# Optimization experiments

Hardware: AMD Instinct MI355X
Metric: run time of the kernel (lower is better)

## Reference

```python
import jax, jax.numpy as jnp
import numpy as np
from jax import lax

K = 3
K2 = K * K
PAD = 1          # dcn padding = kernel_size // 2
OFF_DIL = 2      # offset conv dilation & padding
GN_GROUPS = 32
EPS = 1e-5


def setup_inputs() -> dict:
    key = jax.random.key(0)
    ks = jax.random.split(key, 4)
    B, C1, C2, H, W = 4, 256, 256, 64, 64
    x = jax.random.normal(ks[0], (B, C1, H, W), jnp.float32)
    # offset conv params (zero-init in module; small random here so deformable
    # sampling is genuinely irregular)
    w_off = jax.random.normal(ks[1], (3 * K2, C1, K, K), jnp.float32) * 0.01
    b_off = jax.random.normal(ks[2], (3 * K2,), jnp.float32) * 0.01
    # dcn weight, bias=False
    w_dcn = jax.random.normal(ks[3], (C2, C1, K, K), jnp.float32) * (1.0 / np.sqrt(C1 * K2))
    gamma = jnp.ones((C2,), jnp.float32)
    beta = jnp.zeros((C2,), jnp.float32)
    return {"x": x, "w_off": w_off, "b_off": b_off, "w_dcn": w_dcn,
            "gamma": gamma, "beta": beta}


def _dcnv2_block(x, w_off, b_off, w_dcn, gamma, beta):
    B, C, H, W = x.shape
    C2 = w_dcn.shape[0]

    # ---- offset/mask prediction: 3x3 conv, dilation=2, padding=2, stride=1 ----
    out_off = lax.conv_general_dilated(
        x, w_off, window_strides=(1, 1), padding=[(OFF_DIL, OFF_DIL)] * 2,
        rhs_dilation=(OFF_DIL, OFF_DIL),
        dimension_numbers=("NCHW", "OIHW", "NCHW"))
    out_off = out_off + b_off[None, :, None, None]

    offset = jnp.nan_to_num(jnp.clip(out_off[:, :2 * K2], -64.0, 64.0))
    mask = jax.nn.sigmoid(out_off[:, 2 * K2:])                     # [B,K2,H,W]

    off = offset.reshape(B, K2, 2, H, W)                            # (dy,dx) pairs per kernel pt
    dy, dx = off[:, :, 0], off[:, :, 1]                             # [B,K2,H,W]

    # ---- sampling positions: p0 + pk + offset (stride=1, pad=1, dil=1) ----
    ii = (jnp.arange(K2) // K).astype(jnp.float32)                  # kernel row
    jj = (jnp.arange(K2) % K).astype(jnp.float32)                   # kernel col
    yo = jnp.arange(H, dtype=jnp.float32)
    xo = jnp.arange(W, dtype=jnp.float32)
    py = yo[None, None, :, None] - PAD + ii[None, :, None, None] + dy   # [B,K2,H,W]
    px = xo[None, None, None, :] - PAD + jj[None, :, None, None] + dx

    y0 = jnp.floor(py)
    x0 = jnp.floor(px)
    wy = py - y0                                                    # frac weights
    wx = px - x0
    y0i = y0.astype(jnp.int32)
    x0i = x0.astype(jnp.int32)

    xf = x.reshape(B, C, H * W)

    def gather(yi, xi):
        # zero outside image (torchvision zero-padding bilinear semantics)
        valid = (yi >= 0) & (yi < H) & (xi >= 0) & (xi < W)
        idx = jnp.clip(yi, 0, H - 1) * W + jnp.clip(xi, 0, W - 1)   # [B,K2,H,W]
        v = jax.vmap(lambda xb, ib: xb[:, ib])(xf, idx.reshape(B, -1))  # [B,C,K2*H*W]
        v = v.reshape(B, C, K2, H, W)
        return v * valid[:, None].astype(x.dtype)

    v00 = gather(y0i, x0i)
    v01 = gather(y0i, x0i + 1)
    v10 = gather(y0i + 1, x0i)
    v11 = gather(y0i + 1, x0i + 1)

    wy_ = wy[:, None]
    wx_ = wx[:, None]
    samp = (v00 * (1 - wy_) * (1 - wx_) + v01 * (1 - wy_) * wx_
            + v10 * wy_ * (1 - wx_) + v11 * wy_ * wx_)              # [B,C,K2,H,W]
    samp = samp * mask[:, None]                                     # modulated (DCNv2)

    out = jnp.einsum("bckhw,dck->bdhw", samp, w_dcn.reshape(C2, C, K2))

    # ---- GroupNorm(32, C2) + SiLU ----
    G = GN_GROUPS
    o = out.reshape(B, G, C2 // G, H, W)
    mu = o.mean(axis=(2, 3, 4), keepdims=True)
    var = o.var(axis=(2, 3, 4), keepdims=True)
    o = (o - mu) * lax.rsqrt(var + EPS)
    out = o.reshape(B, C2, H, W) * gamma[None, :, None, None] + beta[None, :, None, None]
    return out * jax.nn.sigmoid(out)


def reference(x, w_off, b_off, w_dcn, gamma, beta):
    return _dcnv2_block(x, w_off, b_off, w_dcn, gamma, beta)
```

## Files before the change

kernel.cpp:

```cpp
#include <hip/hip_runtime.h>
#include <math.h>

#define HW 4096

typedef __attribute__((ext_vector_type(8))) short short8;
typedef __attribute__((ext_vector_type(4))) float f32x4;

static __device__ inline ushort f2bf(float f) {
    uint u = __builtin_bit_cast(uint, f);
    return (ushort)((u + 0x7fffu + ((u >> 16) & 1u)) >> 16);
}
static __device__ inline float lof(uint u) { return __builtin_bit_cast(float, u << 16); }
static __device__ inline float hif(uint u) { return __builtin_bit_cast(float, u & 0xffff0000u); }

__global__ __launch_bounds__(256) void k0_xt(const float* __restrict__ x, ushort* __restrict__ xt)
{
    const int blk = blockIdx.x;
    const int b = blk >> 7, h = (blk & 127) >> 1, ch = blk & 1;
    __shared__ ushort tile[64 * 130];
    const float* xb = x + ((size_t)(b * 256 + ch * 128)) * HW + h * 64;
    const int t = threadIdx.x;
    for (int e = t; e < 8192; e += 256) {
        const int c = e >> 6, j = e & 63;
        tile[j * 130 + c] = f2bf(xb[c * HW + j]);
    }
    __syncthreads();
    for (int e = t; e < 4096; e += 256) {
        const int j = e >> 6, q = e & 63;
        uint* xo = (uint*)(xt + ((size_t)b * HW + h * 64 + j) * 256 + ch * 128);
        xo[q] = *(const uint*)&tile[j * 130 + 2 * q];
    }
}

__global__ __launch_bounds__(256) void k0_w(const float* __restrict__ w_dcn,
    const float* __restrict__ w_off, ushort* __restrict__ wT, ushort* __restrict__ wA)
{
    const int bid = blockIdx.x;
    const int t = threadIdx.x;
    if (bid < 256) {
        const int d = bid;
        __shared__ float wl[2304];
        for (int i = t; i < 2304; i += 256) wl[i] = w_dcn[d * 2304 + i];
        __syncthreads();
        for (int i = t; i < 2304; i += 256) {
            const int k = i >> 8, c = i & 255;
            wT[k * 65536 + d * 256 + c] = f2bf(wl[c * 9 + k]);
        }
    } else {
        const int e = (bid - 256) * 256 + t;
        const int k = e >> 13, r = e & 8191;
        const int oc = r >> 8, c = r & 255;
        wA[e] = f2bf(oc < 27 ? w_off[(oc * 256 + c) * 9 + k] : 0.f);
    }
}

__global__ __launch_bounds__(512) void k1_mfma(const ushort* __restrict__ xt,
    const ushort* __restrict__ wA, const float* __restrict__ b_off,
    float* __restrict__ offs, float* __restrict__ mk)
{
    const int bid = blockIdx.x;
    const int b = bid >> 7, rr_ = bid & 127, h = rr_ >> 1, wh = rr_ & 1;
    const int t = threadIdx.x;
    const int lane = t & 63, wv = t >> 6;
    const int wq = wv & 1, cq = wv >> 1;
    const int n = lane & 15, kq = lane >> 4;
    __shared__ float red[2][3][64][8];

    f32x4 acc0 = {0.f, 0.f, 0.f, 0.f}, acc1 = {0.f, 0.f, 0.f, 0.f};
    const ushort* xb = xt + ((size_t)b * HW) * 256;
    const int wcol = wh * 32 + wq * 16 + n;
    const int cb = cq * 64 + kq * 8;

#pragma unroll
    for (int k = 0; k < 9; ++k) {
        const int i = k / 3, j = k % 3;
        const int hh = h + 2 * (i - 1);
        const int ww = wcol + 2 * (j - 1);
        const bool ok = ((unsigned)hh < 64u) && ((unsigned)ww < 64u);
        const int hc = min(max(hh, 0), 63), wc = min(max(ww, 0), 63);
        const ushort* xrow = xb + (hc * 64 + wc) * 256 + cb;
        const ushort* wr0 = wA + (k * 32 + n) * 256 + cb;
#pragma unroll
        for (int c0 = 0; c0 < 64; c0 += 32) {
            short8 bv = *(const short8*)(xrow + c0);
            if (!ok) bv = (short8){0, 0, 0, 0, 0, 0, 0, 0};
            const short8 a0 = *(const short8*)(wr0 + c0);
            const short8 a1 = *(const short8*)(wr0 + 16 * 256 + c0);
            acc0 = __builtin_amdgcn_mfma_f32_16x16x32_bf16(a0, bv, acc0, 0, 0, 0);
            acc1 = __builtin_amdgcn_mfma_f32_16x16x32_bf16(a1, bv, acc1, 0, 0, 0);
        }
    }

    if (cq > 0) {
#pragma unroll
        for (int r = 0; r < 4; ++r) {
            red[wq][cq - 1][lane][r]     = acc0[r];
            red[wq][cq - 1][lane][4 + r] = acc1[r];
        }
    }
    __syncthreads();
    if (cq == 0) {
#pragma unroll
        for (int p = 0; p < 3; ++p)
#pragma unroll
            for (int r = 0; r < 4; ++r) {
                acc0[r] += red[wq][p][lane][r];
                acc1[r] += red[wq][p][lane][4 + r];
            }
        const int hw = h * 64 + wcol;
#pragma unroll
        for (int r = 0; r < 4; ++r) {
            {
                const int oc = kq * 4 + r;
                float v = acc0[r] + b_off[oc];
                v = fminf(fmaxf(v, -64.f), 64.f);
                offs[(b * 18 + oc) * HW + hw] = v;
            }
            {
                const int oc = 16 + kq * 4 + r;
                const float v = acc1[r] + b_off[min(oc, 26)];
                if (oc < 18) {
                    offs[(b * 18 + oc) * HW + hw] = fminf(fmaxf(v, -64.f), 64.f);
                } else if (oc < 27) {
                    mk[(b * 9 + (oc - 18)) * HW + hw] = 1.f / (1.f + expf(-v));
                }
            }
        }
    }
}

__global__ __launch_bounds__(256) void k2_dcn(const ushort* __restrict__ xt, const ushort* __restrict__ wT,
    const float* __restrict__ offs, const float* __restrict__ mk, float* __restrict__ out)
{
    const int bid = blockIdx.x;
    const int wg = (bid & 7) * 64 + (bid >> 3);
    const int b = wg >> 7, h = (wg & 127) >> 1, wh = wg & 1;
    const int t = threadIdx.x;
    const int lane = t & 63, wv = t >> 6;
    const int n0 = lane & 15, kq = lane >> 4;
    const int d0 = wv * 64;

    __shared__ __align__(16) ushort S[2][8192];
    __shared__ int4   cOff[288];
    __shared__ float4 cWgt[288];

    for (int e = t; e < 288; e += 256) {
        const int k = e >> 5, sl = e & 31, w = wh * 32 + sl;
        const float dy = offs[((size_t)b * 18 + 2 * k) * HW + h * 64 + w];
        const float dx = offs[((size_t)b * 18 + 2 * k + 1) * HW + h * 64 + w];
        const float mval = mk[((size_t)b * 9 + k) * HW + h * 64 + w];
        const float py = (float)(h - 1 + k / 3) + dy;
        const float px = (float)(w - 1 + k % 3) + dx;
        const float y0f = floorf(py), x0f = floorf(px);
        const float wy = py - y0f, wx = px - x0f;
        const int y0 = (int)y0f, x0 = (int)x0f;
        float w00 = (1.f - wy) * (1.f - wx) * mval, w01 = (1.f - wy) * wx * mval;
        float w10 = wy * (1.f - wx) * mval,         w11 = wy * wx * mval;
        const bool vy0 = (unsigned)y0 < 64u, vy1 = (unsigned)(y0 + 1) < 64u;
        const bool vx0 = (unsigned)x0 < 64u, vx1 = (unsigned)(x0 + 1) < 64u;
        if (!(vy0 && vx0)) w00 = 0.f;
        if (!(vy0 && vx1)) w01 = 0.f;
        if (!(vy1 && vx0)) w10 = 0.f;
        if (!(vy1 && vx1)) w11 = 0.f;
        const int y0c = min(max(y0, 0), 63), y1c = min(max(y0 + 1, 0), 63);
        const int x0c = min(max(x0, 0), 63), x1c = min(max(x0 + 1, 0), 63);
        cOff[e] = make_int4((y0c * 64 + x0c) * 512, (y0c * 64 + x1c) * 512,
                            (y1c * 64 + x0c) * 512, (y1c * 64 + x1c) * 512);
        cWgt[e] = make_float4(w00, w01, w10, w11);
    }

    f32x4 acc[4][2];
#pragma unroll
    for (int df = 0; df < 4; ++df)
#pragma unroll
        for (int nf = 0; nf < 2; ++nf) acc[df][nf] = (f32x4){0.f, 0.f, 0.f, 0.f};

    const char* xc = (const char*)(xt + ((size_t)b * HW) * 256);
    const int sl = t >> 3, tj = t & 7;
    const int w7 = sl & 7;

    auto stage = [&](int k, int pb) {
        const int4   co = cOff[k * 32 + sl];
        const float4 cw = cWgt[k * 32 + sl];
        ushort* Sr = &S[pb][sl * 256];
#pragma unroll
        for (int j = 0; j < 4; ++j) {
            const int oct = tj + 8 * j;
            const int cb2 = oct * 16;
            const uint4 v00 = *(const uint4*)(xc + co.x + cb2);
            const uint4 v01 = *(const uint4*)(xc + co.y + cb2);
            const uint4 v10 = *(const uint4*)(xc + co.z + cb2);
            const uint4 v11 = *(const uint4*)(xc + co.w + cb2);
            const uint a00[4] = {v00.x, v00.y, v00.z, v00.w};
            const uint a01[4] = {v01.x, v01.y, v01.z, v01.w};
            const uint a10[4] = {v10.x, v10.y, v10.z, v10.w};
            const uint a11[4] = {v11.x, v11.y, v11.z, v11.w};
            uint r[4];
#pragma unroll
            for (int q = 0; q < 4; ++q) {
                float lo = cw.x * lof(a00[q]);
                lo = fmaf(cw.y, lof(a01[q]), lo);
                lo = fmaf(cw.z, lof(a10[q]), lo);
                lo = fmaf(cw.w, lof(a11[q]), lo);
                float hi = cw.x * hif(a00[q]);
                hi = fmaf(cw.y, hif(a01[q]), hi);
                hi = fmaf(cw.z, hif(a10[q]), hi);
                hi = fmaf(cw.w, hif(a11[q]), hi);
                asm("v_cvt_pk_bf16_f32 %0, %1, %2" : "=v"(r[q]) : "v"(lo), "v"(hi));
            }
            uint4 rv = {r[0], r[1], r[2], r[3]};
            *(uint4*)(Sr + ((oct ^ w7) << 3)) = rv;
        }
    };

    auto gemm = [&](int k, int pb) {
        const ushort* A = wT + k * 65536 + (d0 + n0) * 256 + kq * 8;
#pragma unroll
        for (int c0 = 0; c0 < 256; c0 += 32) {
            short8 a[4];
#pragma unroll
            for (int df = 0; df < 4; ++df)
                a[df] = *(const short8*)(A + df * 4096 + c0);
            const int g0 = (c0 >> 3) + kq;
#pragma unroll
            for (int nf = 0; nf < 2; ++nf) {
                const int wl = nf * 16 + n0;
                const short8 bf = *(const short8*)&S[pb][wl * 256 + ((g0 ^ (wl & 7)) << 3)];
#pragma unroll
                for (int df = 0; df < 4; ++df)
                    acc[df][nf] = __builtin_amdgcn_mfma_f32_16x16x32_bf16(a[df], bf, acc[df][nf], 0, 0, 0);
            }
        }
    };

    __syncthreads();
    stage(0, 0);
    __syncthreads();
#pragma unroll 1
    for (int k = 0; k < 9; ++k) {
        if (k < 8) stage(k + 1, (k + 1) & 1);
        gemm(k, k & 1);
        __syncthreads();
    }

    float* ob = out + ((size_t)b * 256) * HW + h * 64 + wh * 32;
#pragma unroll
    for (int df = 0; df < 4; ++df)
#pragma unroll
        for (int nf = 0; nf < 2; ++nf)
#pragma unroll
            for (int r = 0; r < 4; ++r) {
                const int d = d0 + df * 16 + kq * 4 + r;
                ob[(size_t)d * HW + nf * 16 + n0] = acc[df][nf][r];
            }
}

__global__ __launch_bounds__(256) void k3_stats(const float* __restrict__ out, float* __restrict__ stats)
{
    const int bg = blockIdx.x;
    const float* p = out + (size_t)bg * 32768;
    float s = 0.f, s2 = 0.f;
    for (int i = threadIdx.x; i < 8192; i += 256) {
        float4 v = ((const float4*)p)[i];
        s  += v.x + v.y + v.z + v.w;
        s2 += v.x * v.x + v.y * v.y + v.z * v.z + v.w * v.w;
    }
    __shared__ float r1[256], r2[256];
    r1[threadIdx.x] = s; r2[threadIdx.x] = s2;
    __syncthreads();
    for (int st = 128; st > 0; st >>= 1) {
        if (threadIdx.x < st) {
            r1[threadIdx.x] += r1[threadIdx.x + st];
            r2[threadIdx.x] += r2[threadIdx.x + st];
        }
        __syncthreads();
    }
    if (threadIdx.x == 0) {
        const float mean = r1[0] / 32768.f;
        const float var  = r2[0] / 32768.f - mean * mean;
        stats[bg * 2]     = mean;
        stats[bg * 2 + 1] = rsqrtf(var + 1e-5f);
    }
}

__global__ __launch_bounds__(256) void k4_gn(float* __restrict__ out,
    const float* __restrict__ stats, const float* __restrict__ gamma, const float* __restrict__ beta)
{
    const int i4 = blockIdx.x * 256 + threadIdx.x;
    const int elem = i4 << 2;
    const int b = elem >> 20;
    const int ch = (elem >> 12) & 255;
    const int g = ch >> 3;
    const float mean = stats[(b * 32 + g) * 2];
    const float rstd = stats[(b * 32 + g) * 2 + 1];
    const float ga = gamma[ch], be = beta[ch];
    float4 v = ((float4*)out)[i4];
    float vv[4] = {v.x, v.y, v.z, v.w};
#pragma unroll
    for (int j = 0; j < 4; ++j) {
        const float o = (vv[j] - mean) * rstd * ga + be;
        vv[j] = o / (1.f + expf(-o));
    }
    ((float4*)out)[i4] = make_float4(vv[0], vv[1], vv[2], vv[3]);
}

extern "C" void kernel_launch(void* const* d_in, const int* in_sizes, int n_in,
                              void* d_out, int out_size, void* d_ws, size_t ws_size,
                              hipStream_t stream)
{
    const float* x     = (const float*)d_in[0];
    const float* w_off = (const float*)d_in[1];
    const float* b_off = (const float*)d_in[2];
    const float* w_dcn = (const float*)d_in[3];
    const float* gamma = (const float*)d_in[4];
    const float* beta  = (const float*)d_in[5];
    float* out = (float*)d_out;

    ushort* xt    = (ushort*)d_ws;
    float*  offs  = (float*)d_ws + 2097152;
    float*  mk    = offs + 294912;
    float*  stats = mk + 147456;
    ushort* wT    = (ushort*)(stats + 256);
    ushort* wA    = wT + 589824;

    hipLaunchKernelGGL(k0_xt,    dim3(512),  dim3(256), 0, stream, x, xt);
    hipLaunchKernelGGL(k0_w,     dim3(544),  dim3(256), 0, stream, w_dcn, w_off, wT, wA);
    hipLaunchKernelGGL(k1_mfma,  dim3(512),  dim3(512), 0, stream, xt, wA, b_off, offs, mk);
    hipLaunchKernelGGL(k2_dcn,   dim3(512),  dim3(256), 0, stream, xt, wT, offs, mk, out);
    hipLaunchKernelGGL(k3_stats, dim3(128),  dim3(256), 0, stream, out, stats);
    hipLaunchKernelGGL(k4_gn,    dim3(4096), dim3(256), 0, stream, out, stats, gamma, beta);
}
```

Before: 204.2 us.

## Restructure DCN and offset conv around 32x32 MFMA with register-fed sampled operand

The deformable conv kernel now has each wave gather and bilinearly interpolate its own B fragment straight into registers, with no shared-memory staging of sampled columns. Weights are pre-packed into an MFMA-friendly interleaved layout and streamed into LDS with global_load_lds. The channel reduction is split across waves and combined through LDS at the end, and the grid now tiles over output-channel quarters and full rows. The offset conv also moves to 32x32x16 MFMA with the same layout. In exchange, each sampled value is re-gathered once per output-channel quarter, which adds redundant gather traffic and interpolation arithmetic.

```diff
diff --git a/kernel.cpp b/kernel.cpp
--- a/kernel.cpp
+++ b/kernel.cpp
@@ -3,8 +3,8 @@
 
 #define HW 4096
 
-typedef __attribute__((ext_vector_type(8))) short short8;
-typedef __attribute__((ext_vector_type(4))) float f32x4;
+typedef __attribute__((ext_vector_type(8)))  short short8;
+typedef __attribute__((ext_vector_type(16))) float f32x16;
 
 static __device__ inline ushort f2bf(float f) {
     uint u = __builtin_bit_cast(uint, f);
@@ -33,7 +33,7 @@
 }
 
 __global__ __launch_bounds__(256) void k0_w(const float* __restrict__ w_dcn,
-    const float* __restrict__ w_off, ushort* __restrict__ wT, ushort* __restrict__ wA)
+    const float* __restrict__ w_off, ushort* __restrict__ wT2, ushort* __restrict__ wA2)
 {
     const int bid = blockIdx.x;
     const int t = threadIdx.x;
@@ -44,111 +44,107 @@
         __syncthreads();
         for (int i = t; i < 2304; i += 256) {
             const int k = i >> 8, c = i & 255;
-            wT[k * 65536 + d * 256 + c] = f2bf(wl[c * 9 + k]);
+            wT2[((k * 32 + (c >> 3)) * 256 + d) * 8 + (c & 7)] = f2bf(wl[c * 9 + k]);
         }
     } else {
         const int e = (bid - 256) * 256 + t;
         const int k = e >> 13, r = e & 8191;
-        const int oc = r >> 8, c = r & 255;
-        wA[e] = f2bf(oc < 27 ? w_off[(oc * 256 + c) * 9 + k] : 0.f);
-    }
-}
-
-__global__ __launch_bounds__(512) void k1_mfma(const ushort* __restrict__ xt,
-    const ushort* __restrict__ wA, const float* __restrict__ b_off,
+        const int g = r >> 8, oc = (r >> 3) & 31, ci = r & 7;
+        const int c = g * 8 + ci;
+        wA2[e] = f2bf(oc < 27 ? w_off[(oc * 256 + c) * 9 + k] : 0.f);
+    }
+}
+
+__global__ __launch_bounds__(256, 4) void k1_mfma(const ushort* __restrict__ xt,
+    const ushort* __restrict__ wA2, const float* __restrict__ b_off,
     float* __restrict__ offs, float* __restrict__ mk)
 {
     const int bid = blockIdx.x;
-    const int b = bid >> 7, rr_ = bid & 127, h = rr_ >> 1, wh = rr_ & 1;
+    const int b = bid >> 7, h = (bid >> 1) & 63, wh = bid & 1;
+    const int t = threadIdx.x;
+    const int lane = t & 63, cq = t >> 6;
+    const int l31 = lane & 31, khi = lane >> 5;
+    const int w = wh * 32 + l31;
+
+    __shared__ float red[3 * 1024];
+
+    f32x16 acc = {};
+    const char* xc = (const char*)(xt + ((size_t)b * HW) * 256);
+
+#pragma unroll 1
+    for (int k = 0; k < 9; ++k) {
+        const int hh = h + 2 * (k / 3 - 1);
+        const int ww = w + 2 * (k % 3 - 1);
+        const bool ok = ((unsigned)hh < 64u) && ((unsigned)ww < 64u);
+        const int base = (min(max(hh, 0), 63) * 64 + min(max(ww, 0), 63)) * 512;
+#pragma unroll
+        for (int j = 0; j < 4; ++j) {
+            const int c0 = cq * 64 + j * 16;
+            const int cb = c0 * 2 + khi * 16;
+            short8 bv = *(const short8*)(xc + base + cb);
+            if (!ok) bv = (short8){0, 0, 0, 0, 0, 0, 0, 0};
+            const short8 av = *(const short8*)(wA2 + ((k * 32 + (c0 >> 3) + khi) * 32 + l31) * 8);
+            acc = __builtin_amdgcn_mfma_f32_32x32x16_bf16(av, bv, acc, 0, 0, 0);
+        }
+    }
+
+    if (cq > 0) {
+#pragma unroll
+        for (int r = 0; r < 16; ++r) red[(cq - 1) * 1024 + lane * 16 + r] = acc[r];
+    }
+    __syncthreads();
+    if (cq == 0) {
+#pragma unroll
+        for (int r = 0; r < 16; ++r) {
+            float v = acc[r] + red[lane * 16 + r] + red[1024 + lane * 16 + r] + red[2048 + lane * 16 + r];
+            const int oc = (r & 3) + 8 * (r >> 2) + 4 * khi;
+            v += b_off[min(oc, 26)];
+            const int hw = h * 64 + w;
+            if (oc < 18) {
+                offs[((size_t)b * 18 + oc) * HW + hw] = fminf(fmaxf(v, -64.f), 64.f);
+            } else if (oc < 27) {
+                mk[((size_t)b * 9 + (oc - 18)) * HW + hw] = 1.f / (1.f + expf(-v));
+            }
+        }
+    }
+}
+
+__global__ __launch_bounds__(512, 4) void k2_dcn(const ushort* __restrict__ xt, const ushort* __restrict__ wT2,
+    const float* __restrict__ offs, const float* __restrict__ mk, float* __restrict__ out)
+{
+    const int bid = blockIdx.x;
+    const int wg = (bid & 7) * 128 + (bid >> 3);
+    const int b = wg >> 8, h = (wg >> 2) & 63, dq = wg & 3;
     const int t = threadIdx.x;
     const int lane = t & 63, wv = t >> 6;
-    const int wq = wv & 1, cq = wv >> 1;
-    const int n = lane & 15, kq = lane >> 4;
-    __shared__ float red[2][3][64][8];
-
-    f32x4 acc0 = {0.f, 0.f, 0.f, 0.f}, acc1 = {0.f, 0.f, 0.f, 0.f};
-    const ushort* xb = xt + ((size_t)b * HW) * 256;
-    const int wcol = wh * 32 + wq * 16 + n;
-    const int cb = cq * 64 + kq * 8;
-
-#pragma unroll
+    const int wgrp = wv >> 2, cq = wv & 3;
+    const int l31 = lane & 31, khi = lane >> 5;
+    const int w = wgrp * 32 + l31;
+
+    __shared__ __align__(16) ushort Alds[16384];
+
+    const char* xc = (const char*)(xt + ((size_t)b * HW) * 256);
+    const float* offb = offs + (size_t)b * 18 * HW + h * 64;
+    const float* mkb  = mk   + (size_t)b *  9 * HW + h * 64;
+
+    f32x16 acc[2] = {{}, {}};
+
+    auto issueA = [&](int k) {
+#pragma unroll
+        for (int r = 0; r < 4; ++r) {
+            const ushort* src = wT2 + ((size_t)k * 8192 + (size_t)(r * 8 + wv) * 256 + dq * 64 + lane) * 8;
+            __builtin_amdgcn_global_load_lds(src, Alds + r * 4096 + t * 8, 16, 0, 0);
+        }
+    };
+
+    issueA(0);
+
+#pragma unroll 1
     for (int k = 0; k < 9; ++k) {
-        const int i = k / 3, j = k % 3;
-        const int hh = h + 2 * (i - 1);
-        const int ww = wcol + 2 * (j - 1);
-        const bool ok = ((unsigned)hh < 64u) && ((unsigned)ww < 64u);
-        const int hc = min(max(hh, 0), 63), wc = min(max(ww, 0), 63);
-        const ushort* xrow = xb + (hc * 64 + wc) * 256 + cb;
-        const ushort* wr0 = wA + (k * 32 + n) * 256 + cb;
-#pragma unroll
-        for (int c0 = 0; c0 < 64; c0 += 32) {
-            short8 bv = *(const short8*)(xrow + c0);
-            if (!ok) bv = (short8){0, 0, 0, 0, 0, 0, 0, 0};
-            const short8 a0 = *(const short8*)(wr0 + c0);
-            const short8 a1 = *(const short8*)(wr0 + 16 * 256 + c0);
-            acc0 = __builtin_amdgcn_mfma_f32_16x16x32_bf16(a0, bv, acc0, 0, 0, 0);
-            acc1 = __builtin_amdgcn_mfma_f32_16x16x32_bf16(a1, bv, acc1, 0, 0, 0);
-        }
-    }
-
-    if (cq > 0) {
-#pragma unroll
-        for (int r = 0; r < 4; ++r) {
-            red[wq][cq - 1][lane][r]     = acc0[r];
-            red[wq][cq - 1][lane][4 + r] = acc1[r];
-        }
-    }
-    __syncthreads();
-    if (cq == 0) {
-#pragma unroll
-        for (int p = 0; p < 3; ++p)
-#pragma unroll
-            for (int r = 0; r < 4; ++r) {
-                acc0[r] += red[wq][p][lane][r];
-                acc1[r] += red[wq][p][lane][4 + r];
-            }
-        const int hw = h * 64 + wcol;
-#pragma unroll
-        for (int r = 0; r < 4; ++r) {
-            {
-                const int oc = kq * 4 + r;
-                float v = acc0[r] + b_off[oc];
-                v = fminf(fmaxf(v, -64.f), 64.f);
-                offs[(b * 18 + oc) * HW + hw] = v;
-            }
-            {
-                const int oc = 16 + kq * 4 + r;
-                const float v = acc1[r] + b_off[min(oc, 26)];
-                if (oc < 18) {
-                    offs[(b * 18 + oc) * HW + hw] = fminf(fmaxf(v, -64.f), 64.f);
-                } else if (oc < 27) {
-                    mk[(b * 9 + (oc - 18)) * HW + hw] = 1.f / (1.f + expf(-v));
-                }
-            }
-        }
-    }
-}
-
-__global__ __launch_bounds__(256) void k2_dcn(const ushort* __restrict__ xt, const ushort* __restrict__ wT,
-    const float* __restrict__ offs, const float* __restrict__ mk, float* __restrict__ out)
-{
-    const int bid = blockIdx.x;
-    const int wg = (bid & 7) * 64 + (bid >> 3);
-    const int b = wg >> 7, h = (wg & 127) >> 1, wh = wg & 1;
-    const int t = threadIdx.x;
-    const int lane = t & 63, wv = t >> 6;
-    const int n0 = lane & 15, kq = lane >> 4;
-    const int d0 = wv * 64;
-
-    __shared__ __align__(16) ushort S[2][8192];
-    __shared__ int4   cOff[288];
-    __shared__ float4 cWgt[288];
-
-    for (int e = t; e < 288; e += 256) {
-        const int k = e >> 5, sl = e & 31, w = wh * 32 + sl;
-        const float dy = offs[((size_t)b * 18 + 2 * k) * HW + h * 64 + w];
-        const float dx = offs[((size_t)b * 18 + 2 * k + 1) * HW + h * 64 + w];
-        const float mval = mk[((size_t)b * 9 + k) * HW + h * 64 + w];
+        __syncthreads();
+        const float dy = offb[(2 * k) * HW + w];
+        const float dx = offb[(2 * k + 1) * HW + w];
+        const float mval = mkb[k * HW + w];
         const float py = (float)(h - 1 + k / 3) + dy;
         const float px = (float)(w - 1 + k % 3) + dx;
         const float y0f = floorf(py), x0f = floorf(px);
@@ -164,95 +160,72 @@
         if (!(vy1 && vx1)) w11 = 0.f;
         const int y0c = min(max(y0, 0), 63), y1c = min(max(y0 + 1, 0), 63);
         const int x0c = min(max(x0, 0), 63), x1c = min(max(x0 + 1, 0), 63);
-        cOff[e] = make_int4((y0c * 64 + x0c) * 512, (y0c * 64 + x1c) * 512,
-                            (y1c * 64 + x0c) * 512, (y1c * 64 + x1c) * 512);
-        cWgt[e] = make_float4(w00, w01, w10, w11);
-    }
-
-    f32x4 acc[4][2];
-#pragma unroll
-    for (int df = 0; df < 4; ++df)
-#pragma unroll
-        for (int nf = 0; nf < 2; ++nf) acc[df][nf] = (f32x4){0.f, 0.f, 0.f, 0.f};
-
-    const char* xc = (const char*)(xt + ((size_t)b * HW) * 256);
-    const int sl = t >> 3, tj = t & 7;
-    const int w7 = sl & 7;
-
-    auto stage = [&](int k, int pb) {
-        const int4   co = cOff[k * 32 + sl];
-        const float4 cw = cWgt[k * 32 + sl];
-        ushort* Sr = &S[pb][sl * 256];
+        const int o00 = (y0c * 64 + x0c) * 512, o01 = (y0c * 64 + x1c) * 512;
+        const int o10 = (y1c * 64 + x0c) * 512, o11 = (y1c * 64 + x1c) * 512;
+
 #pragma unroll
         for (int j = 0; j < 4; ++j) {
-            const int oct = tj + 8 * j;
-            const int cb2 = oct * 16;
-            const uint4 v00 = *(const uint4*)(xc + co.x + cb2);
-            const uint4 v01 = *(const uint4*)(xc + co.y + cb2);
-            const uint4 v10 = *(const uint4*)(xc + co.z + cb2);
-            const uint4 v11 = *(const uint4*)(xc + co.w + cb2);
+            const int c0 = cq * 64 + j * 16;
+            const int cb = c0 * 2 + khi * 16;
+            const uint4 v00 = *(const uint4*)(xc + o00 + cb);
+            const uint4 v01 = *(const uint4*)(xc + o01 + cb);
+            const uint4 v10 = *(const uint4*)(xc + o10 + cb);
+            const uint4 v11 = *(const uint4*)(xc + o11 + cb);
             const uint a00[4] = {v00.x, v00.y, v00.z, v00.w};
             const uint a01[4] = {v01.x, v01.y, v01.z, v01.w};
             const uint a10[4] = {v10.x, v10.y, v10.z, v10.w};
             const uint a11[4] = {v11.x, v11.y, v11.z, v11.w};
-            uint r[4];
+            uint rq[4];
 #pragma unroll
             for (int q = 0; q < 4; ++q) {
-                float lo = cw.x * lof(a00[q]);
-                lo = fmaf(cw.y, lof(a01[q]), lo);
-                lo = fmaf(cw.z, lof(a10[q]), lo);
-                lo = fmaf(cw.w, lof(a11[q]), lo);
-                float hi = cw.x * hif(a00[q]);
-                hi = fmaf(cw.y, hif(a01[q]), hi);
-                hi = fmaf(cw.z, hif(a10[q]), hi);
-                hi = fmaf(cw.w, hif(a11[q]), hi);
-                asm("v_cvt_pk_bf16_f32 %0, %1, %2" : "=v"(r[q]) : "v"(lo), "v"(hi));
+                float lo = w00 * lof(a00[q]);
+                lo = fmaf(w01, lof(a01[q]), lo);
+                lo = fmaf(w10, lof(a10[q]), lo);
+                lo = fmaf(w11, lof(a11[q]), lo);
+                float hi = w00 * hif(a00[q]);
+                hi = fmaf(w01, hif(a01[q]), hi);
+                hi = fmaf(w10, hif(a10[q]), hi);
+                hi = fmaf(w11, hif(a11[q]), hi);
+                asm("v_cvt_pk_bf16_f32 %0, %1, %2" : "=v"(rq[q]) : "v"(lo), "v"(hi));
             }
-            uint4 rv = {r[0], r[1], r[2], r[3]};
-            *(uint4*)(Sr + ((oct ^ w7) << 3)) = rv;
-        }
-    };
-
-    auto gemm = [&](int k, int pb) {
-        const ushort* A = wT + k * 65536 + (d0 + n0) * 256 + kq * 8;
-#pragma unroll
-        for (int c0 = 0; c0 < 256; c0 += 32) {
-            short8 a[4];
-#pragma unroll
-            for (int df = 0; df < 4; ++df)
-                a[df] = *(const short8*)(A + df * 4096 + c0);
-            const int g0 = (c0 >> 3) + kq;
-#pragma unroll
-            for (int nf = 0; nf < 2; ++nf) {
-                const int wl = nf * 16 + n0;
-                const short8 bf = *(const short8*)&S[pb][wl * 256 + ((g0 ^ (wl & 7)) << 3)];
-#pragma unroll
-                for (int df = 0; df < 4; ++df)
-                    acc[df][nf] = __builtin_amdgcn_mfma_f32_16x16x32_bf16(a[df], bf, acc[df][nf], 0, 0, 0);
+            short8 bfrag;
+#pragma unroll
+            for (int q = 0; q < 4; ++q) {
+                bfrag[2 * q]     = (short)(rq[q] & 0xffffu);
+                bfrag[2 * q + 1] = (short)(rq[q] >> 16);
             }
-        }
-    };
-
-    __syncthreads();
-    stage(0, 0);
-    __syncthreads();
+            const int gk = cq * 8 + j * 2 + khi;
+            const short8 a0 = *(const short8*)(Alds + (gk * 64 + l31) * 8);
+            const short8 a1 = *(const short8*)(Alds + (gk * 64 + 32 + l31) * 8);
+            acc[0] = __builtin_amdgcn_mfma_f32_32x32x16_bf16(a0, bfrag, acc[0], 0, 0, 0);
+            acc[1] = __builtin_amdgcn_mfma_f32_32x32x16_bf16(a1, bfrag, acc[1], 0, 0, 0);
+        }
+        __syncthreads();
+        if (k < 8) issueA(k + 1);
+    }
+
+    float* redf = (float*)Alds;
+    float* ob = out + ((size_t)b * 256) * HW + h * 64;
 #pragma unroll 1
-    for (int k = 0; k < 9; ++k) {
-        if (k < 8) stage(k + 1, (k + 1) & 1);
-        gemm(k, k & 1);
-        __syncthreads();
-    }
-
-    float* ob = out + ((size_t)b * 256) * HW + h * 64 + wh * 32;
-#pragma unroll
-    for (int df = 0; df < 4; ++df)
-#pragma unroll
-        for (int nf = 0; nf < 2; ++nf)
-#pragma unroll
-            for (int r = 0; r < 4; ++r) {
-                const int d = d0 + df * 16 + kq * 4 + r;
-                ob[(size_t)d * HW + nf * 16 + n0] = acc[df][nf][r];
+    for (int df = 0; df < 2; ++df) {
+        __syncthreads();
+        if (cq > 0) {
+#pragma unroll
+            for (int r = 0; r < 16; ++r)
+                redf[((cq - 1) * 2 + wgrp) * 1024 + lane * 16 + r] = acc[df][r];
+        }
+        __syncthreads();
+        if (cq == 0) {
+#pragma unroll
+            for (int r = 0; r < 16; ++r) {
+                const float v = acc[df][r] + redf[wgrp * 1024 + lane * 16 + r]
+                              + redf[(2 + wgrp) * 1024 + lane * 16 + r]
+                              + redf[(4 + wgrp) * 1024 + lane * 16 + r];
+                const int d = dq * 64 + df * 32 + (r & 3) + 8 * (r >> 2) + 4 * khi;
+                ob[(size_t)d * HW + w] = v;
             }
+        }
+    }
 }
 
 __global__ __launch_bounds__(256) void k3_stats(const float* __restrict__ out, float* __restrict__ stats)
@@ -320,13 +293,13 @@
     float*  offs  = (float*)d_ws + 2097152;
     float*  mk    = offs + 294912;
     float*  stats = mk + 147456;
-    ushort* wT    = (ushort*)(stats + 256);
-    ushort* wA    = wT + 589824;
+    ushort* wT2   = (ushort*)(stats + 256);
+    ushort* wA2   = wT2 + 589824;
 
     hipLaunchKernelGGL(k0_xt,    dim3(512),  dim3(256), 0, stream, x, xt);
-    hipLaunchKernelGGL(k0_w,     dim3(544),  dim3(256), 0, stream, w_dcn, w_off, wT, wA);
-    hipLaunchKernelGGL(k1_mfma,  dim3(512),  dim3(512), 0, stream, xt, wA, b_off, offs, mk);
-    hipLaunchKernelGGL(k2_dcn,   dim3(512),  dim3(256), 0, stream, xt, wT, offs, mk, out);
+    hipLaunchKernelGGL(k0_w,     dim3(544),  dim3(256), 0, stream, w_dcn, w_off, wT2, wA2);
+    hipLaunchKernelGGL(k1_mfma,  dim3(512),  dim3(256), 0, stream, xt, wA2, b_off, offs, mk);
+    hipLaunchKernelGGL(k2_dcn,   dim3(1024), dim3(512), 0, stream, xt, wT2, offs, mk, out);
     hipLaunchKernelGGL(k3_stats, dim3(128),  dim3(256), 0, stream, out, stats);
     hipLaunchKernelGGL(k4_gn,    dim3(4096), dim3(256), 0, stream, out, stats, gamma, beta);
 }
```

Measured after the change: 395.5 us. +93.6%, slower.
